# Performance work log

Measured on AMD Instinct MI355X. Metric: run time of the kernel, lower is better.

The kernel has to match this reference:

```python
import jax, jax.numpy as jnp
import numpy as np

STATE_DIM, ACTION_DIM, HIDDEN_DIM = 512, 64, 2048
INPUT_DIM = STATE_DIM + ACTION_DIM + 1  # 577
BATCH = 4096


def setup_inputs() -> dict:
    key = jax.random.key(0)
    ks = jax.random.split(key, 12)
    sc_x = 1.0 / np.sqrt(INPUT_DIM)
    sc_h = 1.0 / np.sqrt(HIDDEN_DIM)
    return {
        "s": jax.random.normal(ks[0], (BATCH, STATE_DIM), jnp.float32),
        "a_prev": jax.random.normal(ks[1], (BATCH, ACTION_DIM), jnp.float32),
        "r_prev": jax.random.normal(ks[2], (BATCH, 1), jnp.float32),
        "h": jnp.zeros((HIDDEN_DIM,), jnp.float32),
        "c": jnp.zeros((HIDDEN_DIM,), jnp.float32),
        # Fused gate weights: columns ordered [i, f, g(c-tilde), o]
        "Wx": jax.random.uniform(ks[3], (INPUT_DIM, 4 * HIDDEN_DIM), jnp.float32, -sc_x, sc_x),
        "Wh": jax.random.uniform(ks[4], (HIDDEN_DIM, 4 * HIDDEN_DIM), jnp.float32, -sc_h, sc_h),
        "bh": jax.random.uniform(ks[5], (4 * HIDDEN_DIM,), jnp.float32, -sc_h, sc_h),
        "Wa": jax.random.uniform(ks[6], (HIDDEN_DIM, ACTION_DIM), jnp.float32, -sc_h, sc_h),
        "ba": jax.random.uniform(ks[7], (ACTION_DIM,), jnp.float32, -sc_h, sc_h),
        "Wv": jax.random.uniform(ks[8], (HIDDEN_DIM, 1), jnp.float32, -sc_h, sc_h),
        "bv": jax.random.uniform(ks[9], (1,), jnp.float32, -sc_h, sc_h),
    }


def reference(s, a_prev, r_prev, h, c, Wx, Wh, bh, Wa, ba, Wv, bv):
    # x: [B, input_dim]
    x = jnp.concatenate([s, a_prev, r_prev], axis=1)
    # Two fused GEMMs replace the 8 separate small linears (same math).
    z = x @ Wx + h @ Wh + bh          # [B, 4H]
    zi, zf, zg, zo = jnp.split(z, 4, axis=-1)
    i = jax.nn.sigmoid(zi)
    f = jax.nn.sigmoid(zf)
    c_new = f * c + i * jnp.tanh(zg)  # [B, H] (c broadcast over batch)
    o = jax.nn.sigmoid(zo)
    h_new = o * jnp.tanh(c_new)       # [B, H]
    probs = jax.nn.softmax(h_new @ Wa + ba, axis=1)  # [B, A]
    v = h_new @ Wv + bv               # [B, 1]
    return (probs, v)
```

## Files before the change

kernel.cpp:

```cpp
#include <hip/hip_runtime.h>
#include <hip/hip_bf16.h>

#define BATCH   4096
#define SDIM    512
#define ADIM    64
#define IDIM    577
#define KP      608
#define NKT     19
#define HDIM    2048
#define ZDIM    8192

typedef __attribute__((ext_vector_type(8))) __bf16 bf16x8;
typedef __attribute__((ext_vector_type(4))) float  accx4;

__global__ __launch_bounds__(256) void prep_kernel(
    const float* __restrict__ s, const float* __restrict__ a_prev,
    const float* __restrict__ r_prev, const float* __restrict__ bh,
    const float* __restrict__ bv, __hip_bfloat16* __restrict__ xb,
    float* __restrict__ zh, float* __restrict__ vout)
{
    const int bid = blockIdx.x;
    const int t = threadIdx.x;
    if (bid < BATCH) {
        const float* srow = s + (size_t)bid * SDIM;
        const float* arow = a_prev + (size_t)bid * ADIM;
        __hip_bfloat16* xrow = xb + (size_t)bid * KP;
        for (int c = t; c < KP; c += 256) {
            float v;
            if (c < SDIM)        v = srow[c];
            else if (c < 576)    v = arow[c - SDIM];
            else if (c == 576)   v = r_prev[bid];
            else                 v = 0.0f;
            xrow[c] = __float2bfloat16(v);
        }
    } else if (bid < BATCH + 32) {
        int j = (bid - BATCH) * 256 + t;
        zh[j] = bh[j];
    } else {
        int i = (bid - BATCH - 32) * 256 + t;
        if (i < BATCH) vout[i] = bv[0];
    }
}

__global__ __launch_bounds__(256) void transpose_wx(
    const float* __restrict__ wx, __hip_bfloat16* __restrict__ wxt)
{
    __shared__ float tile[32][33];
    const int kt = blockIdx.x;
    const int nt = blockIdx.y;
    const int c  = threadIdx.x & 31;
    const int r0 = threadIdx.x >> 5;
#pragma unroll
    for (int i = 0; i < 4; ++i) {
        int r = r0 + i * 8;
        int k = kt * 32 + r;
        tile[r][c] = (k < IDIM) ? wx[(size_t)k * ZDIM + nt * 32 + c] : 0.0f;
    }
    __syncthreads();
#pragma unroll
    for (int i = 0; i < 4; ++i) {
        int r = r0 + i * 8;
        wxt[(size_t)(nt * 32 + r) * KP + kt * 32 + c] =
            __float2bfloat16(tile[c][r]);
    }
}

__global__ __launch_bounds__(256) void transpose_wa(
    const float* __restrict__ wa, __hip_bfloat16* __restrict__ waT)
{
    __shared__ float tile[32][33];
    const int kt = blockIdx.x;
    const int at = blockIdx.y;
    const int c  = threadIdx.x & 31;
    const int r0 = threadIdx.x >> 5;
#pragma unroll
    for (int i = 0; i < 4; ++i) {
        int r = r0 + i * 8;
        tile[r][c] = wa[(size_t)(kt * 32 + r) * ADIM + at * 32 + c];
    }
    __syncthreads();
#pragma unroll
    for (int i = 0; i < 4; ++i) {
        int r = r0 + i * 8;
        waT[(size_t)(at * 32 + r) * HDIM + kt * 32 + c] =
            __float2bfloat16(tile[c][r]);
    }
}

__global__ __launch_bounds__(256) void zh_acc(
    const float* __restrict__ h, const float* __restrict__ wh,
    float* __restrict__ zh)
{
    const int n  = blockIdx.x * 256 + threadIdx.x;
    const int kb = blockIdx.y * 128;
    float p = 0.0f;
    for (int kk = 0; kk < 128; ++kk)
        p = fmaf(h[kb + kk], wh[(size_t)(kb + kk) * ZDIM + n], p);
    atomicAdd(&zh[n], p);
}

__device__ __forceinline__ float sigmoid_f(float x) {
    return 1.0f / (1.0f + __expf(-x));
}
__device__ __forceinline__ float tanh_f(float x) {
    return 1.0f - 2.0f / (1.0f + __expf(2.0f * x));
}

__global__ __launch_bounds__(256) void lstm_gemm(
    const __hip_bfloat16* __restrict__ xb,
    const __hip_bfloat16* __restrict__ wxt,
    const float* __restrict__ zh,
    const float* __restrict__ cvec,
    const float* __restrict__ wv,
    __hip_bfloat16* __restrict__ hout,
    float* __restrict__ vout)
{
    __shared__ __bf16 smA[128 * 32];
    __shared__ __bf16 smB[128 * 32];
    const int t     = threadIdx.x;
    const int lane  = t & 63;
    const int wid   = t >> 6;
    const int m0    = blockIdx.x * 128;
    const int n0    = blockIdx.y * 32;

    accx4 acc[4][4] = {};

    const int srow   = lane >> 2;
    const int schunk = lane & 3;

    for (int kt = 0; kt < NKT; ++kt) {
        __syncthreads();
        const int kbase = kt * 32 + schunk * 8;
#pragma unroll
        for (int is = 0; is < 2; ++is) {
            const int r = is * 64 + wid * 16 + srow;
            const __hip_bfloat16* ga = xb + (size_t)(m0 + r) * KP + kbase;
            __bf16* la = smA + (is * 64 + wid * 16) * 32;
            __builtin_amdgcn_global_load_lds(
                (const __attribute__((address_space(1))) void*)ga,
                (__attribute__((address_space(3))) void*)la, 16, 0, 0);
            const int g = r >> 5, nn = r & 31;
            const __hip_bfloat16* gb =
                wxt + (size_t)(g * HDIM + n0 + nn) * KP + kbase;
            __bf16* lb = smB + (is * 64 + wid * 16) * 32;
            __builtin_amdgcn_global_load_lds(
                (const __attribute__((address_space(1))) void*)gb,
                (__attribute__((address_space(3))) void*)lb, 16, 0, 0);
        }
        __syncthreads();

        const int wm = wid >> 1, wn = wid & 1;
        const int koff = (lane >> 4) * 8;
        bf16x8 af[4], bfr[4];
#pragma unroll
        for (int rt = 0; rt < 4; ++rt)
            af[rt] = *(const bf16x8*)(smA +
                (wm * 64 + rt * 16 + (lane & 15)) * 32 + koff);
#pragma unroll
        for (int g = 0; g < 4; ++g)
            bfr[g] = *(const bf16x8*)(smB +
                (g * 32 + wn * 16 + (lane & 15)) * 32 + koff);
#pragma unroll
        for (int g = 0; g < 4; ++g)
#pragma unroll
            for (int rt = 0; rt < 4; ++rt)
                acc[g][rt] = __builtin_amdgcn_mfma_f32_16x16x32_bf16(
                    af[rt], bfr[g], acc[g][rt], 0, 0, 0);
    }

    const int wm = wid >> 1, wn = wid & 1;
    const int colg = n0 + wn * 16 + (lane & 15);
    const float cv  = cvec[colg];
    const float wvv = wv[colg];
    const float zhi = zh[colg];
    const float zhf = zh[HDIM + colg];
    const float zhg = zh[2 * HDIM + colg];
    const float zho = zh[3 * HDIM + colg];
#pragma unroll
    for (int rt = 0; rt < 4; ++rt) {
#pragma unroll
        for (int r = 0; r < 4; ++r) {
            const int row = m0 + wm * 64 + rt * 16 + ((lane >> 4) << 2) + r;
            const float zi = acc[0][rt][r] + zhi;
            const float zf = acc[1][rt][r] + zhf;
            const float zg = acc[2][rt][r] + zhg;
            const float zo = acc[3][rt][r] + zho;
            const float cn = sigmoid_f(zf) * cv + sigmoid_f(zi) * tanh_f(zg);
            const float hn = sigmoid_f(zo) * tanh_f(cn);
            hout[(size_t)row * HDIM + colg] = __float2bfloat16(hn);
            float vp = hn * wvv;
            vp += __shfl_xor(vp, 1);
            vp += __shfl_xor(vp, 2);
            vp += __shfl_xor(vp, 4);
            vp += __shfl_xor(vp, 8);
            if ((lane & 15) == 0) atomicAdd(&vout[row], vp);
        }
    }
}

__global__ __launch_bounds__(256) void head_kernel(
    const __hip_bfloat16* __restrict__ hnew,
    const __hip_bfloat16* __restrict__ waT,
    const float* __restrict__ ba, float* __restrict__ probs)
{
    __shared__ float lg[16][68];
    const int t    = threadIdx.x;
    const int lane = t & 63;
    const int wid  = t >> 6;
    const int r0   = blockIdx.x * 16;

    const __bf16* arow = (const __bf16*)hnew +
        (size_t)(r0 + (lane & 15)) * HDIM + (lane >> 4) * 8;
    const __bf16* brow = (const __bf16*)waT +
        (size_t)(wid * 16 + (lane & 15)) * HDIM + (lane >> 4) * 8;

    accx4 acc = {};
#pragma unroll 8
    for (int kk = 0; kk < HDIM; kk += 32) {
        bf16x8 af = *(const bf16x8*)(arow + kk);
        bf16x8 bf = *(const bf16x8*)(brow + kk);
        acc = __builtin_amdgcn_mfma_f32_16x16x32_bf16(af, bf, acc, 0, 0, 0);
    }
#pragma unroll
    for (int r = 0; r < 4; ++r)
        lg[(lane >> 4) * 4 + r][wid * 16 + (lane & 15)] = acc[r];
    __syncthreads();

    const float bav = ba[lane];
#pragma unroll
    for (int i = 0; i < 4; ++i) {
        const int row = wid * 4 + i;
        const float logit = lg[row][lane] + bav;
        float m = logit;
#pragma unroll
        for (int mask = 32; mask >= 1; mask >>= 1)
            m = fmaxf(m, __shfl_xor(m, mask));
        const float e = __expf(logit - m);
        float ssum = e;
#pragma unroll
        for (int mask = 32; mask >= 1; mask >>= 1)
            ssum += __shfl_xor(ssum, mask);
        probs[(size_t)(r0 + row) * 64 + lane] = e / ssum;
    }
}

extern "C" void kernel_launch(void* const* d_in, const int* in_sizes, int n_in,
                              void* d_out, int out_size, void* d_ws,
                              size_t ws_size, hipStream_t stream)
{
    const float* s      = (const float*)d_in[0];
    const float* a_prev = (const float*)d_in[1];
    const float* r_prev = (const float*)d_in[2];
    const float* h      = (const float*)d_in[3];
    const float* c      = (const float*)d_in[4];
    const float* Wx     = (const float*)d_in[5];
    const float* Wh     = (const float*)d_in[6];
    const float* bh     = (const float*)d_in[7];
    const float* Wa     = (const float*)d_in[8];
    const float* ba     = (const float*)d_in[9];
    const float* Wv     = (const float*)d_in[10];
    const float* bv     = (const float*)d_in[11];

    float* out   = (float*)d_out;
    float* probs = out;
    float* vout  = out + (size_t)BATCH * ADIM;

    char* ws = (char*)d_ws;
    __hip_bfloat16* xb   = (__hip_bfloat16*)ws;
    __hip_bfloat16* wxt  = (__hip_bfloat16*)(ws + 4980736);
    float* zh            = (float*)(ws + 14942208);
    __hip_bfloat16* hnew = (__hip_bfloat16*)(ws + 14974976);
    __hip_bfloat16* waT  = (__hip_bfloat16*)(ws + 31752192);

    prep_kernel<<<BATCH + 32 + 16, 256, 0, stream>>>(
        s, a_prev, r_prev, bh, bv, xb, zh, vout);
    transpose_wx<<<dim3(NKT, 256), 256, 0, stream>>>(Wx, wxt);
    transpose_wa<<<dim3(HDIM / 32, ADIM / 32), 256, 0, stream>>>(Wa, waT);
    zh_acc<<<dim3(32, 16), 256, 0, stream>>>(h, Wh, zh);
    lstm_gemm<<<dim3(BATCH / 128, HDIM / 32), 256, 0, stream>>>(
        xb, wxt, zh, c, Wv, hnew, vout);
    head_kernel<<<BATCH / 16, 256, 0, stream>>>(hnew, waT, ba, probs);
}
```

Measured before the change: 241.6 us.

## Merge setup kernels, widen GEMM K-tile with swizzle, move value head into head kernel

Merges the four preprocessing launches (x conversion, Wx/Wa transposes, Wh·h partial sums) into one setup kernel. The Wh·h partials are written to eight slices and reduced in the GEMM epilogue, which removes the bias-init pass and the atomics. The LSTM GEMM now uses a 64-wide K tile with an XOR-swizzled LDS layout and K padded to 640, halving the barrier count per block. The value projection moves from per-row atomics in the GEMM epilogue into a 512-thread head kernel that splits K across two wave groups. This trades launch overhead and atomic traffic for extra epilogue loads and some redundant padded K work.

```diff
diff --git a/kernel.cpp b/kernel.cpp
--- a/kernel.cpp
+++ b/kernel.cpp
@@ -5,98 +5,85 @@
 #define SDIM    512
 #define ADIM    64
 #define IDIM    577
-#define KP      608
-#define NKT     19
+#define KP2     640
+#define NKT2    10
 #define HDIM    2048
 #define ZDIM    8192
 
 typedef __attribute__((ext_vector_type(8))) __bf16 bf16x8;
 typedef __attribute__((ext_vector_type(4))) float  accx4;
 
-__global__ __launch_bounds__(256) void prep_kernel(
+__global__ __launch_bounds__(256) void setup_kernel(
     const float* __restrict__ s, const float* __restrict__ a_prev,
-    const float* __restrict__ r_prev, const float* __restrict__ bh,
-    const float* __restrict__ bv, __hip_bfloat16* __restrict__ xb,
-    float* __restrict__ zh, float* __restrict__ vout)
-{
+    const float* __restrict__ r_prev, const float* __restrict__ h,
+    const float* __restrict__ wx, const float* __restrict__ wh,
+    const float* __restrict__ wa,
+    __hip_bfloat16* __restrict__ xb, __hip_bfloat16* __restrict__ wxt,
+    __hip_bfloat16* __restrict__ waT, float* __restrict__ zh_w)
+{
+    __shared__ float stile[64 * 33];
     const int bid = blockIdx.x;
     const int t = threadIdx.x;
-    if (bid < BATCH) {
-        const float* srow = s + (size_t)bid * SDIM;
-        const float* arow = a_prev + (size_t)bid * ADIM;
-        __hip_bfloat16* xrow = xb + (size_t)bid * KP;
-        for (int c = t; c < KP; c += 256) {
+
+    if (bid < 2560) {
+        const int kt2 = bid >> 8;
+        const int nt  = bid & 255;
+        const int c  = t & 31, r0 = t >> 5;
+#pragma unroll
+        for (int i = 0; i < 8; ++i) {
+            int r = r0 + i * 8;
+            int k = kt2 * 64 + r;
+            stile[r * 33 + c] =
+                (k < IDIM) ? wx[(size_t)k * ZDIM + nt * 32 + c] : 0.0f;
+        }
+        __syncthreads();
+        const int nr = t >> 3, ch = t & 7;
+        bf16x8 w8;
+#pragma unroll
+        for (int j = 0; j < 8; ++j)
+            w8[j] = (__bf16)stile[(ch * 8 + j) * 33 + nr];
+        *(bf16x8*)(wxt + (size_t)(nt * 32 + nr) * KP2 + kt2 * 64 + ch * 8) = w8;
+    } else if (bid < 2816) {
+        const int zb = bid - 2560;
+        const int nb = zb & 31, ky = zb >> 5;
+        const int n  = nb * 256 + t;
+        const float* hp  = h + ky * 256;
+        const float* whp = wh + (size_t)ky * 256 * ZDIM + n;
+        float p = 0.0f;
+#pragma unroll 8
+        for (int kk = 0; kk < 256; ++kk)
+            p = fmaf(hp[kk], whp[(size_t)kk * ZDIM], p);
+        zh_w[ky * ZDIM + n] = p;
+    } else if (bid < 6912) {
+        const int row = bid - 2816;
+        const float* srow = s + (size_t)row * SDIM;
+        const float* arow = a_prev + (size_t)row * ADIM;
+        __hip_bfloat16* xrow = xb + (size_t)row * KP2;
+        for (int c = t; c < KP2; c += 256) {
             float v;
             if (c < SDIM)        v = srow[c];
             else if (c < 576)    v = arow[c - SDIM];
-            else if (c == 576)   v = r_prev[bid];
+            else if (c == 576)   v = r_prev[row];
             else                 v = 0.0f;
             xrow[c] = __float2bfloat16(v);
         }
-    } else if (bid < BATCH + 32) {
-        int j = (bid - BATCH) * 256 + t;
-        zh[j] = bh[j];
     } else {
-        int i = (bid - BATCH - 32) * 256 + t;
-        if (i < BATCH) vout[i] = bv[0];
-    }
-}
-
-__global__ __launch_bounds__(256) void transpose_wx(
-    const float* __restrict__ wx, __hip_bfloat16* __restrict__ wxt)
-{
-    __shared__ float tile[32][33];
-    const int kt = blockIdx.x;
-    const int nt = blockIdx.y;
-    const int c  = threadIdx.x & 31;
-    const int r0 = threadIdx.x >> 5;
-#pragma unroll
-    for (int i = 0; i < 4; ++i) {
-        int r = r0 + i * 8;
-        int k = kt * 32 + r;
-        tile[r][c] = (k < IDIM) ? wx[(size_t)k * ZDIM + nt * 32 + c] : 0.0f;
-    }
-    __syncthreads();
-#pragma unroll
-    for (int i = 0; i < 4; ++i) {
-        int r = r0 + i * 8;
-        wxt[(size_t)(nt * 32 + r) * KP + kt * 32 + c] =
-            __float2bfloat16(tile[c][r]);
-    }
-}
-
-__global__ __launch_bounds__(256) void transpose_wa(
-    const float* __restrict__ wa, __hip_bfloat16* __restrict__ waT)
-{
-    __shared__ float tile[32][33];
-    const int kt = blockIdx.x;
-    const int at = blockIdx.y;
-    const int c  = threadIdx.x & 31;
-    const int r0 = threadIdx.x >> 5;
-#pragma unroll
-    for (int i = 0; i < 4; ++i) {
-        int r = r0 + i * 8;
-        tile[r][c] = wa[(size_t)(kt * 32 + r) * ADIM + at * 32 + c];
-    }
-    __syncthreads();
-#pragma unroll
-    for (int i = 0; i < 4; ++i) {
-        int r = r0 + i * 8;
-        waT[(size_t)(at * 32 + r) * HDIM + kt * 32 + c] =
-            __float2bfloat16(tile[c][r]);
-    }
-}
-
-__global__ __launch_bounds__(256) void zh_acc(
-    const float* __restrict__ h, const float* __restrict__ wh,
-    float* __restrict__ zh)
-{
-    const int n  = blockIdx.x * 256 + threadIdx.x;
-    const int kb = blockIdx.y * 128;
-    float p = 0.0f;
-    for (int kk = 0; kk < 128; ++kk)
-        p = fmaf(h[kb + kk], wh[(size_t)(kb + kk) * ZDIM + n], p);
-    atomicAdd(&zh[n], p);
+        const int wb = bid - 6912;
+        const int kt = wb >> 1, at = wb & 1;
+        const int c  = t & 31, r0 = t >> 5;
+#pragma unroll
+        for (int i = 0; i < 4; ++i) {
+            int r = r0 + i * 8;
+            stile[r * 33 + c] = wa[(size_t)(kt * 32 + r) * ADIM + at * 32 + c];
+        }
+        __syncthreads();
+#pragma unroll
+        for (int i = 0; i < 4; ++i) {
+            int r = r0 + i * 8;
+            waT[(size_t)(at * 32 + r) * HDIM + kt * 32 + c] =
+                __float2bfloat16(stile[c * 33 + r]);
+        }
+    }
 }
 
 __device__ __forceinline__ float sigmoid_f(float x) {
@@ -109,128 +96,155 @@
 __global__ __launch_bounds__(256) void lstm_gemm(
     const __hip_bfloat16* __restrict__ xb,
     const __hip_bfloat16* __restrict__ wxt,
-    const float* __restrict__ zh,
+    const float* __restrict__ zh_w,
+    const float* __restrict__ bh,
     const float* __restrict__ cvec,
-    const float* __restrict__ wv,
-    __hip_bfloat16* __restrict__ hout,
-    float* __restrict__ vout)
-{
-    __shared__ __bf16 smA[128 * 32];
-    __shared__ __bf16 smB[128 * 32];
-    const int t     = threadIdx.x;
-    const int lane  = t & 63;
-    const int wid   = t >> 6;
-    const int m0    = blockIdx.x * 128;
-    const int n0    = blockIdx.y * 32;
+    __hip_bfloat16* __restrict__ hout)
+{
+    __shared__ __bf16 smA[128 * 64];
+    __shared__ __bf16 smB[128 * 64];
+    const int t    = threadIdx.x;
+    const int lane = t & 63;
+    const int wid  = t >> 6;
+    const int m0   = blockIdx.x * 128;
+    const int n0   = blockIdx.y * 32;
 
     accx4 acc[4][4] = {};
 
-    const int srow   = lane >> 2;
-    const int schunk = lane & 3;
-
-    for (int kt = 0; kt < NKT; ++kt) {
-        __syncthreads();
-        const int kbase = kt * 32 + schunk * 8;
-#pragma unroll
-        for (int is = 0; is < 2; ++is) {
-            const int r = is * 64 + wid * 16 + srow;
-            const __hip_bfloat16* ga = xb + (size_t)(m0 + r) * KP + kbase;
-            __bf16* la = smA + (is * 64 + wid * 16) * 32;
+    const int srow = lane >> 3;
+    const int slot = lane & 7;
+    const int wm = wid >> 1, wn = wid & 1;
+    const int fl15 = lane & 15;
+    const int fhi  = lane >> 4;
+
+    for (int kt = 0; kt < NKT2; ++kt) {
+        __syncthreads();
+#pragma unroll
+        for (int i = 0; i < 4; ++i) {
+            const int r = wid * 32 + i * 8 + srow;
+            const int c = slot ^ (r & 7);
+            const __hip_bfloat16* ga =
+                xb + (size_t)(m0 + r) * KP2 + kt * 64 + c * 8;
+            __bf16* la = smA + (wid * 32 + i * 8) * 64;
             __builtin_amdgcn_global_load_lds(
                 (const __attribute__((address_space(1))) void*)ga,
                 (__attribute__((address_space(3))) void*)la, 16, 0, 0);
             const int g = r >> 5, nn = r & 31;
             const __hip_bfloat16* gb =
-                wxt + (size_t)(g * HDIM + n0 + nn) * KP + kbase;
-            __bf16* lb = smB + (is * 64 + wid * 16) * 32;
+                wxt + (size_t)(g * HDIM + n0 + nn) * KP2 + kt * 64 + c * 8;
+            __bf16* lb = smB + (wid * 32 + i * 8) * 64;
             __builtin_amdgcn_global_load_lds(
                 (const __attribute__((address_space(1))) void*)gb,
                 (__attribute__((address_space(3))) void*)lb, 16, 0, 0);
         }
         __syncthreads();
 
-        const int wm = wid >> 1, wn = wid & 1;
-        const int koff = (lane >> 4) * 8;
-        bf16x8 af[4], bfr[4];
-#pragma unroll
-        for (int rt = 0; rt < 4; ++rt)
-            af[rt] = *(const bf16x8*)(smA +
-                (wm * 64 + rt * 16 + (lane & 15)) * 32 + koff);
-#pragma unroll
-        for (int g = 0; g < 4; ++g)
-            bfr[g] = *(const bf16x8*)(smB +
-                (g * 32 + wn * 16 + (lane & 15)) * 32 + koff);
-#pragma unroll
-        for (int g = 0; g < 4; ++g)
+#pragma unroll
+        for (int hf = 0; hf < 2; ++hf) {
+            const int ck = hf * 4 + fhi;
+            const int sl = (ck ^ (lane & 7)) * 8;
+            bf16x8 af[4], bfr[4];
 #pragma unroll
             for (int rt = 0; rt < 4; ++rt)
-                acc[g][rt] = __builtin_amdgcn_mfma_f32_16x16x32_bf16(
-                    af[rt], bfr[g], acc[g][rt], 0, 0, 0);
-    }
-
-    const int wm = wid >> 1, wn = wid & 1;
-    const int colg = n0 + wn * 16 + (lane & 15);
-    const float cv  = cvec[colg];
-    const float wvv = wv[colg];
-    const float zhi = zh[colg];
-    const float zhf = zh[HDIM + colg];
-    const float zhg = zh[2 * HDIM + colg];
-    const float zho = zh[3 * HDIM + colg];
+                af[rt] = *(const bf16x8*)(smA +
+                    (wm * 64 + rt * 16 + fl15) * 64 + sl);
+#pragma unroll
+            for (int g = 0; g < 4; ++g)
+                bfr[g] = *(const bf16x8*)(smB +
+                    (g * 32 + wn * 16 + fl15) * 64 + sl);
+#pragma unroll
+            for (int g = 0; g < 4; ++g)
+#pragma unroll
+                for (int rt = 0; rt < 4; ++rt)
+                    acc[g][rt] = __builtin_amdgcn_mfma_f32_16x16x32_bf16(
+                        af[rt], bfr[g], acc[g][rt], 0, 0, 0);
+        }
+    }
+
+    const int colg = n0 + wn * 16 + fl15;
+    float zsum[4];
+#pragma unroll
+    for (int g = 0; g < 4; ++g) {
+        float v = bh[g * HDIM + colg];
+#pragma unroll
+        for (int j = 0; j < 8; ++j)
+            v += zh_w[j * ZDIM + g * HDIM + colg];
+        zsum[g] = v;
+    }
+    const float cv = cvec[colg];
 #pragma unroll
     for (int rt = 0; rt < 4; ++rt) {
 #pragma unroll
         for (int r = 0; r < 4; ++r) {
-            const int row = m0 + wm * 64 + rt * 16 + ((lane >> 4) << 2) + r;
-            const float zi = acc[0][rt][r] + zhi;
-            const float zf = acc[1][rt][r] + zhf;
-            const float zg = acc[2][rt][r] + zhg;
-            const float zo = acc[3][rt][r] + zho;
+            const int row = m0 + wm * 64 + rt * 16 + (fhi << 2) + r;
+            const float zi = acc[0][rt][r] + zsum[0];
+            const float zf = acc[1][rt][r] + zsum[1];
+            const float zg = acc[2][rt][r] + zsum[2];
+            const float zo = acc[3][rt][r] + zsum[3];
             const float cn = sigmoid_f(zf) * cv + sigmoid_f(zi) * tanh_f(zg);
             const float hn = sigmoid_f(zo) * tanh_f(cn);
             hout[(size_t)row * HDIM + colg] = __float2bfloat16(hn);
-            float vp = hn * wvv;
-            vp += __shfl_xor(vp, 1);
-            vp += __shfl_xor(vp, 2);
-            vp += __shfl_xor(vp, 4);
-            vp += __shfl_xor(vp, 8);
-            if ((lane & 15) == 0) atomicAdd(&vout[row], vp);
-        }
-    }
-}
-
-__global__ __launch_bounds__(256) void head_kernel(
+        }
+    }
+}
+
+__global__ __launch_bounds__(512) void head_kernel(
     const __hip_bfloat16* __restrict__ hnew,
     const __hip_bfloat16* __restrict__ waT,
-    const float* __restrict__ ba, float* __restrict__ probs)
-{
-    __shared__ float lg[16][68];
+    const float* __restrict__ wv,
+    const float* __restrict__ ba, const float* __restrict__ bv,
+    float* __restrict__ probs, float* __restrict__ vout)
+{
+    __shared__ float lg[2][16][68];
+    __shared__ float vpart[2][16];
     const int t    = threadIdx.x;
     const int lane = t & 63;
     const int wid  = t >> 6;
+    const int kh   = wid >> 2;
+    const int wid2 = wid & 3;
     const int r0   = blockIdx.x * 16;
+    const int fl15 = lane & 15, fhi = lane >> 4;
 
     const __bf16* arow = (const __bf16*)hnew +
-        (size_t)(r0 + (lane & 15)) * HDIM + (lane >> 4) * 8;
+        (size_t)(r0 + fl15) * HDIM + kh * 1024 + fhi * 8;
     const __bf16* brow = (const __bf16*)waT +
-        (size_t)(wid * 16 + (lane & 15)) * HDIM + (lane >> 4) * 8;
-
-    accx4 acc = {};
-#pragma unroll 8
-    for (int kk = 0; kk < HDIM; kk += 32) {
-        bf16x8 af = *(const bf16x8*)(arow + kk);
-        bf16x8 bf = *(const bf16x8*)(brow + kk);
-        acc = __builtin_amdgcn_mfma_f32_16x16x32_bf16(af, bf, acc, 0, 0, 0);
+        (size_t)(wid2 * 16 + fl15) * HDIM + kh * 1024 + fhi * 8;
+    const float* wvp = wv + kh * 1024 + fhi * 8;
+    const bool do_v = (wid2 == 0);
+
+    accx4 acc0 = {}, acc1 = {};
+    float vacc = 0.0f;
+#pragma unroll 4
+    for (int kk = 0; kk < 1024; kk += 64) {
+        bf16x8 a0 = *(const bf16x8*)(arow + kk);
+        bf16x8 b0 = *(const bf16x8*)(brow + kk);
+        bf16x8 a1 = *(const bf16x8*)(arow + kk + 32);
+        bf16x8 b1 = *(const bf16x8*)(brow + kk + 32);
+        acc0 = __builtin_amdgcn_mfma_f32_16x16x32_bf16(a0, b0, acc0, 0, 0, 0);
+        acc1 = __builtin_amdgcn_mfma_f32_16x16x32_bf16(a1, b1, acc1, 0, 0, 0);
+        if (do_v) {
+#pragma unroll
+            for (int j = 0; j < 8; ++j) {
+                vacc = fmaf((float)a0[j], wvp[kk + j], vacc);
+                vacc = fmaf((float)a1[j], wvp[kk + 32 + j], vacc);
+            }
+        }
     }
 #pragma unroll
     for (int r = 0; r < 4; ++r)
-        lg[(lane >> 4) * 4 + r][wid * 16 + (lane & 15)] = acc[r];
+        lg[kh][fhi * 4 + r][wid2 * 16 + fl15] = acc0[r] + acc1[r];
+    if (do_v) {
+        vacc += __shfl_xor(vacc, 16);
+        vacc += __shfl_xor(vacc, 32);
+        if (lane < 16) vpart[kh][lane] = vacc;
+    }
     __syncthreads();
 
     const float bav = ba[lane];
 #pragma unroll
-    for (int i = 0; i < 4; ++i) {
-        const int row = wid * 4 + i;
-        const float logit = lg[row][lane] + bav;
+    for (int i = 0; i < 2; ++i) {
+        const int row = wid * 2 + i;
+        const float logit = lg[0][row][lane] + lg[1][row][lane] + bav;
         float m = logit;
 #pragma unroll
         for (int mask = 32; mask >= 1; mask >>= 1)
@@ -242,6 +256,7 @@
             ssum += __shfl_xor(ssum, mask);
         probs[(size_t)(r0 + row) * 64 + lane] = e / ssum;
     }
+    if (t < 16) vout[r0 + t] = vpart[0][t] + vpart[1][t] + bv[0];
 }
 
 extern "C" void kernel_launch(void* const* d_in, const int* in_sizes, int n_in,
@@ -267,17 +282,15 @@
 
     char* ws = (char*)d_ws;
     __hip_bfloat16* xb   = (__hip_bfloat16*)ws;
-    __hip_bfloat16* wxt  = (__hip_bfloat16*)(ws + 4980736);
-    float* zh            = (float*)(ws + 14942208);
-    __hip_bfloat16* hnew = (__hip_bfloat16*)(ws + 14974976);
-    __hip_bfloat16* waT  = (__hip_bfloat16*)(ws + 31752192);
-
-    prep_kernel<<<BATCH + 32 + 16, 256, 0, stream>>>(
-        s, a_prev, r_prev, bh, bv, xb, zh, vout);
-    transpose_wx<<<dim3(NKT, 256), 256, 0, stream>>>(Wx, wxt);
-    transpose_wa<<<dim3(HDIM / 32, ADIM / 32), 256, 0, stream>>>(Wa, waT);
-    zh_acc<<<dim3(32, 16), 256, 0, stream>>>(h, Wh, zh);
+    __hip_bfloat16* wxt  = (__hip_bfloat16*)(ws + 5242880);
+    __hip_bfloat16* waT  = (__hip_bfloat16*)(ws + 15728640);
+    float* zh_w          = (float*)(ws + 15990784);
+    __hip_bfloat16* hnew = (__hip_bfloat16*)(ws + 16252928);
+
+    setup_kernel<<<7040, 256, 0, stream>>>(
+        s, a_prev, r_prev, h, Wx, Wh, Wa, xb, wxt, waT, zh_w);
     lstm_gemm<<<dim3(BATCH / 128, HDIM / 32), 256, 0, stream>>>(
-        xb, wxt, zh, c, Wv, hnew, vout);
-    head_kernel<<<BATCH / 16, 256, 0, stream>>>(hnew, waT, ba, probs);
-}
+        xb, wxt, zh_w, bh, c, hnew);
+    head_kernel<<<BATCH / 16, 512, 0, stream>>>(
+        hnew, waT, Wv, ba, bv, probs, vout);
+}
```

Result: faster. 235.8 us (-2.4%).
